# Kernel tuning notes

Measured on AMD Instinct MI355X. Metric: run time of the kernel, lower is better.

Reference implementation:

```python
import jax, jax.numpy as jnp
import numpy as np

B, S, HID, H = 2, 2048, 1024, 16
D = HID // H
LAMBDA_INIT = 0.8
GN_EPS = 1e-5


def setup_inputs() -> dict:
    rng = jax.random.key(0)
    ks = jax.random.split(rng, 12)
    w = 0.02
    return {
        "query": jax.random.normal(ks[0], (B, S, HID), dtype=jnp.float32),
        "key": jax.random.normal(ks[1], (B, S, HID), dtype=jnp.float32),
        "value": jax.random.normal(ks[2], (B, S, HID), dtype=jnp.float32),
        "attention_mask": jnp.ones((B, S), dtype=jnp.float32),
        # params ([in, out] layout; x @ W)
        "Wq": jax.random.normal(ks[3], (HID, H * D * 2), dtype=jnp.float32) * w,
        "Wk": jax.random.normal(ks[4], (HID, H * D * 2), dtype=jnp.float32) * w,
        "Wv": jax.random.normal(ks[5], (HID, H * D), dtype=jnp.float32) * w,
        "Wo": jax.random.normal(ks[6], (H * D, HID), dtype=jnp.float32) * w,
        "lam_q1": jax.random.normal(ks[7], (D,), dtype=jnp.float32),
        "lam_q2": jax.random.normal(ks[8], (D,), dtype=jnp.float32),
        "lam_k1": jax.random.normal(ks[9], (D,), dtype=jnp.float32),
        "lam_k2": jax.random.normal(ks[10], (D,), dtype=jnp.float32),
        "gn_weight": jnp.ones((H * D,), dtype=jnp.float32),
        "gn_bias": jnp.zeros((H * D,), dtype=jnp.float32),
    }


def reference(query, key, value, attention_mask, Wq, Wk, Wv, Wo,
              lam_q1, lam_q2, lam_k1, lam_k2, gn_weight, gn_bias):
    b, s, hid = query.shape
    h, d = H, hid // H
    rs = 1.0 / jnp.sqrt(jnp.asarray(d, query.dtype))

    q = (query @ Wq).reshape(b, s, h, 2 * d).transpose(0, 2, 1, 3)   # [b,h,s,2d]
    k = (key @ Wk).reshape(b, s, h, 2 * d).transpose(0, 2, 1, 3)
    v = (value @ Wv).reshape(b, s, h, d).transpose(0, 2, 1, 3)       # [b,h,s,d]

    Q1, Q2 = q[..., :d], q[..., d:]
    K1, K2 = k[..., :d], k[..., d:]
    s1 = jnp.einsum('bhqd,bhkd->bhqk', Q1, K1) * rs
    s2 = jnp.einsum('bhqd,bhkd->bhqk', Q2, K2) * rs

    # ALiBi bias: slopes[h] * (pos_q - pos_k), subtracted from scores
    pos = jnp.arange(s, dtype=query.dtype)
    slopes = 2.0 ** (-8.0 * jnp.arange(1, h + 1, dtype=query.dtype) / h)
    alibi = slopes[None, :, None, None] * (pos[:, None] - pos[None, :])[None, None]
    causal = jnp.triu(jnp.full((s, s), -1e9, dtype=query.dtype), k=1)[None, None]
    pad = (1.0 - attention_mask)[:, None, None, :] * -1e9
    add = -alibi + causal + pad

    w1 = jax.nn.softmax(s1 + add, axis=-1)
    w2 = jax.nn.softmax(s2 + add, axis=-1)

    lam = (jnp.exp(jnp.dot(lam_q1, lam_k1))
           - jnp.exp(jnp.dot(lam_q2, lam_k2)) + LAMBDA_INIT)
    dw = w1 - lam * w2

    attn = jnp.einsum('bhqk,bhkd->bhqd', dw, v).transpose(0, 2, 1, 3)  # [b,s,h,d]

    # GroupNorm(groups=h, channels=h*d) over [b, C, L]: per (b, head) normalize over (seq, d)
    mean = attn.mean(axis=(1, 3), keepdims=True)
    var = ((attn - mean) ** 2).mean(axis=(1, 3), keepdims=True)
    normed = (attn - mean) / jnp.sqrt(var + GN_EPS)
    normed = normed * gn_weight.reshape(1, 1, h, d) + gn_bias.reshape(1, 1, h, d)

    out = normed * (1.0 - LAMBDA_INIT)
    return out.reshape(b, s, h * d) @ Wo
```

## Files before the change

kernel.cpp:

```cpp
#include <hip/hip_runtime.h>
#include <cstdint>
#include <cstddef>

#define SQ 2048
#define NH 16
#define DH 64
#define HIDN 1024

typedef __attribute__((ext_vector_type(8))) short bf16x8;
typedef __attribute__((ext_vector_type(4))) float f32x4;
typedef __attribute__((ext_vector_type(2))) unsigned u32x2;

__device__ inline short f2b(float x) {
  union { float f; unsigned u; } un; un.f = x;
  unsigned r = un.u + 0x7fffu + ((un.u >> 16) & 1u);
  return (short)(r >> 16);
}

__device__ inline unsigned cvt_pk(float lo, float hi) {
  unsigned r;
  asm("v_cvt_pk_bf16_f32 %0, %1, %2" : "=v"(r) : "v"(lo), "v"(hi));
  return r;
}

__device__ inline f32x4 mfma16(u32x2 a, u32x2 b, f32x4 c) {
  asm("v_mfma_f32_16x16x16_bf16 %0, %1, %2, %0" : "+v"(c) : "v"(a), "v"(b));
  return c;
}

__device__ inline void gl_lds16(const void* g, void* l) {
  __builtin_amdgcn_global_load_lds(
      (const __attribute__((address_space(1))) void*)g,
      (__attribute__((address_space(3))) void*)l, 16, 0, 0);
}

__global__ __launch_bounds__(256) void qkv_to_bf16(const float4* __restrict__ q,
                                                   const float4* __restrict__ k,
                                                   const float4* __restrict__ v,
                                                   short4* __restrict__ out) {
  int i = blockIdx.x * 256 + threadIdx.x;
  const float4* src = (i < 1048576) ? q : ((i < 2097152) ? k : v);
  float4 val = src[i & 1048575];
  short4 o;
  o.x = f2b(val.x); o.y = f2b(val.y); o.z = f2b(val.z); o.w = f2b(val.w);
  out[i] = o;
}

__global__ __launch_bounds__(256) void wconv4(const float* __restrict__ Wq,
                                              const float* __restrict__ Wk,
                                              const float* __restrict__ Wv,
                                              const float* __restrict__ Wo,
                                              short* __restrict__ WqT, short* __restrict__ WkT,
                                              short* __restrict__ WvT, short* __restrict__ WoT) {
  __shared__ float t[32][33];
  int z = blockIdx.z;
  int N = (z < 2) ? 2048 : 1024;
  if (blockIdx.x * 32 >= N) return;
  const float* W = (z == 0) ? Wq : (z == 1) ? Wk : (z == 2) ? Wv : Wo;
  short* Wt = (z == 0) ? WqT : (z == 1) ? WkT : (z == 2) ? WvT : WoT;
  const int K = 1024;
  int n0 = blockIdx.x * 32, k0 = blockIdx.y * 32;
  int tx = threadIdx.x & 31, ty = threadIdx.x >> 5;
#pragma unroll
  for (int r = 0; r < 4; ++r)
    t[ty + r * 8][tx] = W[(size_t)(k0 + ty + r * 8) * N + n0 + tx];
  __syncthreads();
#pragma unroll
  for (int r = 0; r < 4; ++r)
    Wt[(size_t)(n0 + ty + r * 8) * K + k0 + tx] = f2b(t[tx][ty + r * 8]);
}

__global__ void lam_k(const float* __restrict__ q1, const float* __restrict__ q2,
                      const float* __restrict__ k1, const float* __restrict__ k2,
                      float* __restrict__ out) {
  int i = threadIdx.x;
  float d1 = q1[i] * k1[i], d2 = q2[i] * k2[i];
#pragma unroll
  for (int x = 1; x < 64; x <<= 1) { d1 += __shfl_xor(d1, x); d2 += __shfl_xor(d2, x); }
  if (i == 0) out[0] = __expf(d1) - __expf(d2) + 0.8f;
}

template <int MODE>
__global__ __launch_bounds__(256) void gemm_bt(const short* __restrict__ A,
                                               const short* __restrict__ Bt,
                                               void* __restrict__ Cout, int N, int K) {
  __shared__ __align__(16) short As[128 * 64];
  __shared__ __align__(16) short Bs[128 * 64];
  const int tid = threadIdx.x;
  const int lane = tid & 63, w = tid >> 6;
  const int l15 = lane & 15, lhi = lane >> 4;
  const int wr = w >> 1, wc = w & 1;
  const int m0 = blockIdx.y * 128, n0 = blockIdx.x * 128;

  f32x4 acc[4][4];
#pragma unroll
  for (int i = 0; i < 4; ++i)
#pragma unroll
    for (int j = 0; j < 4; ++j) acc[i][j] = (f32x4){0.f, 0.f, 0.f, 0.f};

  const short* Ag = A + (size_t)m0 * K;
  const short* Bg = Bt + (size_t)n0 * K;

  for (int k0 = 0; k0 < K; k0 += 64) {
#pragma unroll
    for (int it = 0; it < 4; ++it) {
      int idx = it * 256 + tid;
      int row = idx >> 3, c8 = (idx & 7) << 3;
      gl_lds16(Ag + (size_t)row * K + (k0 + c8), &As[idx << 3]);
      gl_lds16(Bg + (size_t)row * K + (k0 + c8), &Bs[idx << 3]);
    }
    __syncthreads();
#pragma unroll
    for (int kk = 0; kk < 64; kk += 32) {
      bf16x8 af[4], bfr[4];
#pragma unroll
      for (int mi = 0; mi < 4; ++mi)
        af[mi] = *(const bf16x8*)&As[(wr * 64 + mi * 16 + l15) * 64 + kk + lhi * 8];
#pragma unroll
      for (int ni = 0; ni < 4; ++ni)
        bfr[ni] = *(const bf16x8*)&Bs[(wc * 64 + ni * 16 + l15) * 64 + kk + lhi * 8];
#pragma unroll
      for (int mi = 0; mi < 4; ++mi)
#pragma unroll
        for (int ni = 0; ni < 4; ++ni)
          acc[mi][ni] = __builtin_amdgcn_mfma_f32_16x16x32_bf16(af[mi], bfr[ni], acc[mi][ni], 0, 0, 0);
    }
    __syncthreads();
  }

#pragma unroll
  for (int mi = 0; mi < 4; ++mi) {
#pragma unroll
    for (int ni = 0; ni < 4; ++ni) {
#pragma unroll
      for (int j = 0; j < 4; ++j) {
        int m = m0 + wr * 64 + mi * 16 + (lhi << 2) + j;
        int n = n0 + wc * 64 + ni * 16 + l15;
        float v = acc[mi][ni][j];
        if (MODE == 0) {
          ((float*)Cout)[(size_t)m * N + n] = v;
        } else if (MODE == 1) {
          int s = m & (SQ - 1), bb = m >> 11;
          int h = n >> 7, t = n & 127, path = t >> 6, tt = t & 63;
          ((short*)Cout)[((((size_t)(bb * NH + h) * 2 + path) * SQ + s) << 6) + tt] = f2b(v);
        } else {
          int s = m & (SQ - 1), bb = m >> 11;
          int h = n >> 6, t = n & 63;
          ((short*)Cout)[(((size_t)(bb * NH + h) << 6) + t) * SQ + s] = f2b(v);
        }
      }
    }
  }
}

__global__ __launch_bounds__(256) void diff_attn(
    const short* __restrict__ Qp, const short* __restrict__ Kp,
    const short* __restrict__ Vt, const float* __restrict__ maskp,
    const float* __restrict__ lamp, float* __restrict__ attn,
    float* __restrict__ part) {
  __shared__ __align__(16) short K1s[64 * 64];
  __shared__ __align__(16) short K2s[64 * 64];
  __shared__ __align__(16) short Vts[64 * 64];
  __shared__ float d_s[2048];
  __shared__ float red[8];

  const int bid = blockIdx.x;
  const int chunk = bid >> 8, c = bid & 255, sub = c >> 5, bh = c & 31;
  int qt;
  if (chunk == 0) qt = 31 - sub;
  else if (chunk == 1) qt = 16 + sub;
  else if (chunk == 2) qt = 15 - sub;
  else qt = sub;

  const int b = bh >> 4, h = bh & 15;
  const int tid = threadIdx.x, lane = tid & 63, w = tid >> 6;
  const int l15 = lane & 15, lhi = lane >> 4;
  const int sw7 = l15 & 7;
  const int u0 = (lhi ^ sw7) << 3, u1 = ((4 + lhi) ^ sw7) << 3;
  const int wq0 = qt * 64 + w * 16;
  const int q = wq0 + l15;
  const float slope = exp2f(-0.5f * (float)(h + 1));
  const float L2E = 1.44269504089f;
  const float SC = 0.125f * L2E;
  const float qb8 = slope * (float)q * L2E + 8.0f;

  for (int i = tid; i < 2048; i += 256)
    d_s[i] = (slope * (float)i + (1.0f - maskp[(b << 11) + i]) * (-1.0e9f)) * L2E;

  const short* Q1g = Qp + (((size_t)bh * 2 + 0) * SQ) * DH;
  const short* Q2g = Qp + (((size_t)bh * 2 + 1) * SQ) * DH;
  const short* K1g = Kp + (((size_t)bh * 2 + 0) * SQ) * DH;
  const short* K2g = Kp + (((size_t)bh * 2 + 1) * SQ) * DH;
  const short* Vtg = Vt + (size_t)bh * DH * SQ;

  bf16x8 aq[2][2];
#pragma unroll
  for (int kk = 0; kk < 2; ++kk) {
    aq[0][kk] = *(const bf16x8*)&Q1g[(size_t)q * DH + kk * 32 + lhi * 8];
    aq[1][kk] = *(const bf16x8*)&Q2g[(size_t)q * DH + kk * 32 + lhi * 8];
  }

  int ucf[4];
#pragma unroll
  for (int cf = 0; cf < 4; ++cf)
    ucf[cf] = (((2 * cf + (lhi >> 1)) ^ sw7) << 1) + (lhi & 1);

  f32x4 acc[2][4];
  float ll[2] = {0.f, 0.f};
#pragma unroll
  for (int p = 0; p < 2; ++p)
#pragma unroll
    for (int i = 0; i < 4; ++i) acc[p][i] = (f32x4){0.f, 0.f, 0.f, 0.f};

  for (int kt = 0; kt <= qt; ++kt) {
    const int k0 = kt * 64;
#pragma unroll
    for (int it = 0; it < 2; ++it) {
      int idx = it * 256 + tid;
      int row = idx >> 3, u = idx & 7;
      int us = (u ^ (row & 7)) << 3;
      gl_lds16(K1g + (size_t)(k0 + row) * DH + us, &K1s[idx << 3]);
      gl_lds16(K2g + (size_t)(k0 + row) * DH + us, &K2s[idx << 3]);
      gl_lds16(Vtg + (size_t)row * SQ + k0 + us, &Vts[idx << 3]);
    }
    __syncthreads();

    f32x4 dvq[4];
#pragma unroll
    for (int cf = 0; cf < 4; ++cf) {
      f32x4 dv = *(const f32x4*)&d_s[k0 + 16 * cf + 4 * lhi];
#pragma unroll
      for (int j = 0; j < 4; ++j) dvq[cf][j] = dv[j] - qb8;
    }
    const bool diag = (kt == qt);

    u32x2 pa[2][4];
#pragma unroll
    for (int p = 0; p < 2; ++p) {
      const short* Ks = (p == 0) ? K1s : K2s;
      f32x4 sv[4];
#pragma unroll
      for (int cf = 0; cf < 4; ++cf) {
        int rb = (cf * 16 + l15) << 6;
        f32x4 z = (f32x4){0.f, 0.f, 0.f, 0.f};
        bf16x8 ka = *(const bf16x8*)&Ks[rb + u0];
        bf16x8 kb = *(const bf16x8*)&Ks[rb + u1];
        sv[cf] = __builtin_amdgcn_mfma_f32_16x16x32_bf16(ka, aq[p][0], z, 0, 0, 0);
        sv[cf] = __builtin_amdgcn_mfma_f32_16x16x32_bf16(kb, aq[p][1], sv[cf], 0, 0, 0);
      }
      float rsum = 0.f;
#pragma unroll
      for (int cf = 0; cf < 4; ++cf) {
        float pv[4];
#pragma unroll
        for (int j = 0; j < 4; ++j) pv[j] = sv[cf][j] * SC + dvq[cf][j];
        if (diag) {
#pragma unroll
          for (int j = 0; j < 4; ++j) {
            int kc = k0 + 16 * cf + 4 * lhi + j;
            pv[j] = (kc > q) ? -1.0e9f : pv[j];
          }
        }
        float e0 = exp2f(pv[0]);
        float e1 = exp2f(pv[1]);
        float e2 = exp2f(pv[2]);
        float e3 = exp2f(pv[3]);
        rsum += (e0 + e1) + (e2 + e3);
        pa[p][cf][0] = cvt_pk(e0, e1);
        pa[p][cf][1] = cvt_pk(e2, e3);
      }
      ll[p] += rsum;
    }

#pragma unroll
    for (int df = 0; df < 4; ++df) {
      const u32x2* vrow = (const u32x2*)&Vts[(df * 16 + l15) << 6];
#pragma unroll
      for (int cf = 0; cf < 4; ++cf) {
        u32x2 vb = vrow[ucf[cf]];
        acc[0][df] = mfma16(pa[0][cf], vb, acc[0][df]);
        acc[1][df] = mfma16(pa[1][cf], vb, acc[1][df]);
      }
    }
    __syncthreads();
  }

#pragma unroll
  for (int p = 0; p < 2; ++p) {
    ll[p] += __shfl_xor(ll[p], 16);
    ll[p] += __shfl_xor(ll[p], 32);
  }
  float lamv = lamp[0];
  float li1 = 1.0f / ll[0], li2 = lamv / ll[1];
  float li1b[4], li2b[4];
#pragma unroll
  for (int j = 0; j < 4; ++j) {
    li1b[j] = __shfl(li1, (lhi << 2) + j);
    li2b[j] = __shfl(li2, (lhi << 2) + j);
  }
  float lsum = 0.f, lsq = 0.f;
#pragma unroll
  for (int df = 0; df < 4; ++df)
#pragma unroll
    for (int j = 0; j < 4; ++j) {
      int qq = wq0 + (lhi << 2) + j;
      float o = acc[0][df][j] * li1b[j] - acc[1][df][j] * li2b[j];
      attn[((size_t)b * SQ + qq) * HIDN + (h << 6) + (df << 4) + l15] = o;
      lsum += o; lsq += o * o;
    }
#pragma unroll
  for (int x = 1; x < 64; x <<= 1) {
    lsum += __shfl_xor(lsum, x);
    lsq += __shfl_xor(lsq, x);
  }
  if (lane == 0) { red[w] = lsum; red[4 + w] = lsq; }
  __syncthreads();
  if (tid == 0) {
    part[((size_t)bh * 32 + qt) * 2] = red[0] + red[1] + red[2] + red[3];
    part[((size_t)bh * 32 + qt) * 2 + 1] = red[4] + red[5] + red[6] + red[7];
  }
}

__global__ void stats_fin(const float* __restrict__ part, float* __restrict__ mi) {
  int bh = threadIdx.x;
  float s = 0.f, ss = 0.f;
  for (int t = 0; t < 32; ++t) {
    s += part[(bh * 32 + t) * 2];
    ss += part[(bh * 32 + t) * 2 + 1];
  }
  float n = (float)(SQ * DH);
  float mean = s / n;
  float var = ss / n - mean * mean;
  mi[bh * 2] = mean;
  mi[bh * 2 + 1] = rsqrtf(var + 1e-5f);
}

__global__ __launch_bounds__(256) void gn_apply(const float* __restrict__ attn,
                                                const float* __restrict__ mi,
                                                const float* __restrict__ gnw,
                                                const float* __restrict__ gnb,
                                                short* __restrict__ X) {
  size_t i = (size_t)blockIdx.x * 256 + threadIdx.x;
  size_t base = i << 2;
  int r = (int)(base >> 10);
  int c = (int)(base & 1023);
  int bh = ((r >> 11) << 4) + (c >> 6);
  float mean = mi[bh * 2], inv = mi[bh * 2 + 1];
  float4 a = *(const float4*)&attn[base];
  short4 o;
  o.x = f2b(((a.x - mean) * inv * gnw[c + 0] + gnb[c + 0]) * 0.2f);
  o.y = f2b(((a.y - mean) * inv * gnw[c + 1] + gnb[c + 1]) * 0.2f);
  o.z = f2b(((a.z - mean) * inv * gnw[c + 2] + gnb[c + 2]) * 0.2f);
  o.w = f2b(((a.w - mean) * inv * gnw[c + 3] + gnb[c + 3]) * 0.2f);
  *(short4*)&X[base] = o;
}

extern "C" void kernel_launch(void* const* d_in, const int* in_sizes, int n_in,
                              void* d_out, int out_size, void* d_ws, size_t ws_size,
                              hipStream_t stream) {
  const float* query = (const float*)d_in[0];
  const float* key = (const float*)d_in[1];
  const float* value = (const float*)d_in[2];
  const float* mask = (const float*)d_in[3];
  const float* Wq = (const float*)d_in[4];
  const float* Wk = (const float*)d_in[5];
  const float* Wv = (const float*)d_in[6];
  const float* Wo = (const float*)d_in[7];
  const float* lq1 = (const float*)d_in[8];
  const float* lq2 = (const float*)d_in[9];
  const float* lk1 = (const float*)d_in[10];
  const float* lk2 = (const float*)d_in[11];
  const float* gnw = (const float*)d_in[12];
  const float* gnb = (const float*)d_in[13];

  char* ws = (char*)d_ws;
  short* WqT = (short*)(ws + 0);
  short* WkT = (short*)(ws + 4194304);
  short* WvT = (short*)(ws + 8388608);
  short* WoT = (short*)(ws + 10485760);
  short* qb = (short*)(ws + 12582912);
  short* kb = (short*)(ws + 20971520);
  short* vb = (short*)(ws + 29360128);
  short* Qp = (short*)(ws + 37748736);
  short* Kp = (short*)(ws + 54525952);
  short* Vtb = (short*)(ws + 71303168);
  float* attn = (float*)(ws + 12582912);
  short* X = (short*)(ws + 29360128);
  float* part = (float*)(ws + 79691776);
  float* mi = (float*)(ws + 79699968);
  float* lam = (float*)(ws + 79700224);

  qkv_to_bf16<<<12288, 256, 0, stream>>>((const float4*)query, (const float4*)key,
                                         (const float4*)value, (short4*)qb);
  wconv4<<<dim3(64, 32, 4), 256, 0, stream>>>(Wq, Wk, Wv, Wo, WqT, WkT, WvT, WoT);
  lam_k<<<1, 64, 0, stream>>>(lq1, lq2, lk1, lk2, lam);

  gemm_bt<1><<<dim3(16, 32), 256, 0, stream>>>(qb, WqT, Qp, 2048, 1024);
  gemm_bt<1><<<dim3(16, 32), 256, 0, stream>>>(kb, WkT, Kp, 2048, 1024);
  gemm_bt<2><<<dim3(8, 32), 256, 0, stream>>>(vb, WvT, Vtb, 1024, 1024);

  diff_attn<<<dim3(1024), 256, 0, stream>>>(Qp, Kp, Vtb, mask, lam, attn, part);
  stats_fin<<<1, 32, 0, stream>>>(part, mi);
  gn_apply<<<4096, 256, 0, stream>>>(attn, mi, gnw, gnb, X);
  gemm_bt<0><<<dim3(8, 32), 256, 0, stream>>>(X, WoT, d_out, 1024, 1024);
}
```

Baseline: 219.6 us.

## Merge QKV projections into one launch and pair query stripes for causal balance

The three projection GEMMs are combined into a single launch using a z-dimension, and the output GEMM becomes its own non-templated kernel. The attention kernel now gives each block two 32-row query stripes, a and 63-a, handled by different wave pairs, so every block does about the same causal work. The GroupNorm partial-statistics buffer doubles to match. Waves on the shorter stripe still wait at each K/V tile barrier until the longer stripe finishes, so some waves sit idle during the tail of each block.

Measured after the change: 267.1 us. +21.6%, slower.

```diff
diff --git a/kernel.cpp b/kernel.cpp
--- a/kernel.cpp
+++ b/kernel.cpp
@@ -80,10 +80,17 @@
   if (i == 0) out[0] = __expf(d1) - __expf(d2) + 0.8f;
 }
 
-template <int MODE>
-__global__ __launch_bounds__(256) void gemm_bt(const short* __restrict__ A,
-                                               const short* __restrict__ Bt,
-                                               void* __restrict__ Cout, int N, int K) {
+__global__ __launch_bounds__(256) void proj3(const short* __restrict__ Abase,
+                                             const short* __restrict__ Btbase,
+                                             short* __restrict__ QKout,
+                                             short* __restrict__ Vtb) {
+  const int z = blockIdx.z;
+  if (z == 2 && blockIdx.x >= 8) return;
+  const int N = (z < 2) ? 2048 : 1024;
+  const int K = 1024;
+  const short* A = Abase + (size_t)z * 4194304;
+  const short* Bt = Btbase + (size_t)z * 2097152;
+
   __shared__ __align__(16) short As[128 * 64];
   __shared__ __align__(16) short Bs[128 * 64];
   const int tid = threadIdx.x;
@@ -137,20 +144,78 @@
         int m = m0 + wr * 64 + mi * 16 + (lhi << 2) + j;
         int n = n0 + wc * 64 + ni * 16 + l15;
         float v = acc[mi][ni][j];
-        if (MODE == 0) {
-          ((float*)Cout)[(size_t)m * N + n] = v;
-        } else if (MODE == 1) {
-          int s = m & (SQ - 1), bb = m >> 11;
+        int s = m & (SQ - 1), bb = m >> 11;
+        if (z < 2) {
           int h = n >> 7, t = n & 127, path = t >> 6, tt = t & 63;
-          ((short*)Cout)[((((size_t)(bb * NH + h) * 2 + path) * SQ + s) << 6) + tt] = f2b(v);
+          (QKout + (size_t)z * 8388608)
+              [((((size_t)(bb * NH + h) * 2 + path) * SQ + s) << 6) + tt] = f2b(v);
         } else {
-          int s = m & (SQ - 1), bb = m >> 11;
           int h = n >> 6, t = n & 63;
-          ((short*)Cout)[(((size_t)(bb * NH + h) << 6) + t) * SQ + s] = f2b(v);
+          Vtb[(((size_t)(bb * NH + h) << 6) + t) * SQ + s] = f2b(v);
         }
       }
     }
   }
+}
+
+__global__ __launch_bounds__(256) void gemm_out(const short* __restrict__ A,
+                                                const short* __restrict__ Bt,
+                                                float* __restrict__ Cout) {
+  const int N = 1024, K = 1024;
+  __shared__ __align__(16) short As[128 * 64];
+  __shared__ __align__(16) short Bs[128 * 64];
+  const int tid = threadIdx.x;
+  const int lane = tid & 63, w = tid >> 6;
+  const int l15 = lane & 15, lhi = lane >> 4;
+  const int wr = w >> 1, wc = w & 1;
+  const int m0 = blockIdx.y * 128, n0 = blockIdx.x * 128;
+
+  f32x4 acc[4][4];
+#pragma unroll
+  for (int i = 0; i < 4; ++i)
+#pragma unroll
+    for (int j = 0; j < 4; ++j) acc[i][j] = (f32x4){0.f, 0.f, 0.f, 0.f};
+
+  const short* Ag = A + (size_t)m0 * K;
+  const short* Bg = Bt + (size_t)n0 * K;
+
+  for (int k0 = 0; k0 < K; k0 += 64) {
+#pragma unroll
+    for (int it = 0; it < 4; ++it) {
+      int idx = it * 256 + tid;
+      int row = idx >> 3, c8 = (idx & 7) << 3;
+      gl_lds16(Ag + (size_t)row * K + (k0 + c8), &As[idx << 3]);
+      gl_lds16(Bg + (size_t)row * K + (k0 + c8), &Bs[idx << 3]);
+    }
+    __syncthreads();
+#pragma unroll
+    for (int kk = 0; kk < 64; kk += 32) {
+      bf16x8 af[4], bfr[4];
+#pragma unroll
+      for (int mi = 0; mi < 4; ++mi)
+        af[mi] = *(const bf16x8*)&As[(wr * 64 + mi * 16 + l15) * 64 + kk + lhi * 8];
+#pragma unroll
+      for (int ni = 0; ni < 4; ++ni)
+        bfr[ni] = *(const bf16x8*)&Bs[(wc * 64 + ni * 16 + l15) * 64 + kk + lhi * 8];
+#pragma unroll
+      for (int mi = 0; mi < 4; ++mi)
+#pragma unroll
+        for (int ni = 0; ni < 4; ++ni)
+          acc[mi][ni] = __builtin_amdgcn_mfma_f32_16x16x32_bf16(af[mi], bfr[ni], acc[mi][ni], 0, 0, 0);
+    }
+    __syncthreads();
+  }
+
+#pragma unroll
+  for (int mi = 0; mi < 4; ++mi)
+#pragma unroll
+    for (int ni = 0; ni < 4; ++ni)
+#pragma unroll
+      for (int j = 0; j < 4; ++j) {
+        int m = m0 + wr * 64 + mi * 16 + (lhi << 2) + j;
+        int n = n0 + wc * 64 + ni * 16 + l15;
+        Cout[(size_t)m * N + n] = acc[mi][ni][j];
+      }
 }
 
 __global__ __launch_bounds__(256) void diff_attn(
@@ -165,20 +230,21 @@
   __shared__ float red[8];
 
   const int bid = blockIdx.x;
-  const int chunk = bid >> 8, c = bid & 255, sub = c >> 5, bh = c & 31;
-  int qt;
-  if (chunk == 0) qt = 31 - sub;
-  else if (chunk == 1) qt = 16 + sub;
-  else if (chunk == 2) qt = 15 - sub;
-  else qt = sub;
+  const int chunk = bid >> 8, cc = bid & 255, sub = cc >> 5, bh = cc & 31;
+  const int a = chunk * 8 + sub;
 
   const int b = bh >> 4, h = bh & 15;
   const int tid = threadIdx.x, lane = tid & 63, w = tid >> 6;
   const int l15 = lane & 15, lhi = lane >> 4;
   const int sw7 = l15 & 7;
   const int u0 = (lhi ^ sw7) << 3, u1 = ((4 + lhi) ^ sw7) << 3;
-  const int wq0 = qt * 64 + w * 16;
+
+  const int st = (w >> 1) ? (63 - a) : a;
+  const int ktmax = st >> 1;
+  const int ktmaxB = (63 - a) >> 1;
+  const int wq0 = st * 32 + (w & 1) * 16;
   const int q = wq0 + l15;
+
   const float slope = exp2f(-0.5f * (float)(h + 1));
   const float L2E = 1.44269504089f;
   const float SC = 0.125f * L2E;
@@ -212,7 +278,7 @@
 #pragma unroll
     for (int i = 0; i < 4; ++i) acc[p][i] = (f32x4){0.f, 0.f, 0.f, 0.f};
 
-  for (int kt = 0; kt <= qt; ++kt) {
+  for (int kt = 0; kt <= ktmaxB; ++kt) {
     const int k0 = kt * 64;
 #pragma unroll
     for (int it = 0; it < 2; ++it) {
@@ -225,61 +291,63 @@
     }
     __syncthreads();
 
-    f32x4 dvq[4];
-#pragma unroll
-    for (int cf = 0; cf < 4; ++cf) {
-      f32x4 dv = *(const f32x4*)&d_s[k0 + 16 * cf + 4 * lhi];
-#pragma unroll
-      for (int j = 0; j < 4; ++j) dvq[cf][j] = dv[j] - qb8;
-    }
-    const bool diag = (kt == qt);
-
-    u32x2 pa[2][4];
-#pragma unroll
-    for (int p = 0; p < 2; ++p) {
-      const short* Ks = (p == 0) ? K1s : K2s;
-      f32x4 sv[4];
+    if (kt <= ktmax) {
+      f32x4 dvq[4];
 #pragma unroll
       for (int cf = 0; cf < 4; ++cf) {
-        int rb = (cf * 16 + l15) << 6;
-        f32x4 z = (f32x4){0.f, 0.f, 0.f, 0.f};
-        bf16x8 ka = *(const bf16x8*)&Ks[rb + u0];
-        bf16x8 kb = *(const bf16x8*)&Ks[rb + u1];
-        sv[cf] = __builtin_amdgcn_mfma_f32_16x16x32_bf16(ka, aq[p][0], z, 0, 0, 0);
-        sv[cf] = __builtin_amdgcn_mfma_f32_16x16x32_bf16(kb, aq[p][1], sv[cf], 0, 0, 0);
+        f32x4 dv = *(const f32x4*)&d_s[k0 + 16 * cf + 4 * lhi];
+#pragma unroll
+        for (int j = 0; j < 4; ++j) dvq[cf][j] = dv[j] - qb8;
       }
-      float rsum = 0.f;
-#pragma unroll
-      for (int cf = 0; cf < 4; ++cf) {
-        float pv[4];
-#pragma unroll
-        for (int j = 0; j < 4; ++j) pv[j] = sv[cf][j] * SC + dvq[cf][j];
-        if (diag) {
-#pragma unroll
-          for (int j = 0; j < 4; ++j) {
-            int kc = k0 + 16 * cf + 4 * lhi + j;
-            pv[j] = (kc > q) ? -1.0e9f : pv[j];
+      const bool diag = (kt == ktmax);
+
+      u32x2 pa[2][4];
+#pragma unroll
+      for (int p = 0; p < 2; ++p) {
+        const short* Ks = (p == 0) ? K1s : K2s;
+        f32x4 sv[4];
+#pragma unroll
+        for (int cf = 0; cf < 4; ++cf) {
+          int rb = (cf * 16 + l15) << 6;
+          f32x4 z = (f32x4){0.f, 0.f, 0.f, 0.f};
+          bf16x8 ka = *(const bf16x8*)&Ks[rb + u0];
+          bf16x8 kb = *(const bf16x8*)&Ks[rb + u1];
+          sv[cf] = __builtin_amdgcn_mfma_f32_16x16x32_bf16(ka, aq[p][0], z, 0, 0, 0);
+          sv[cf] = __builtin_amdgcn_mfma_f32_16x16x32_bf16(kb, aq[p][1], sv[cf], 0, 0, 0);
+        }
+        float rsum = 0.f;
+#pragma unroll
+        for (int cf = 0; cf < 4; ++cf) {
+          float pv[4];
+#pragma unroll
+          for (int j = 0; j < 4; ++j) pv[j] = sv[cf][j] * SC + dvq[cf][j];
+          if (diag) {
+#pragma unroll
+            for (int j = 0; j < 4; ++j) {
+              int kc = k0 + 16 * cf + 4 * lhi + j;
+              pv[j] = (kc > q) ? -1.0e9f : pv[j];
+            }
           }
+          float e0 = exp2f(pv[0]);
+          float e1 = exp2f(pv[1]);
+          float e2 = exp2f(pv[2]);
+          float e3 = exp2f(pv[3]);
+          rsum += (e0 + e1) + (e2 + e3);
+          pa[p][cf][0] = cvt_pk(e0, e1);
+          pa[p][cf][1] = cvt_pk(e2, e3);
         }
-        float e0 = exp2f(pv[0]);
-        float e1 = exp2f(pv[1]);
-        float e2 = exp2f(pv[2]);
-        float e3 = exp2f(pv[3]);
-        rsum += (e0 + e1) + (e2 + e3);
-        pa[p][cf][0] = cvt_pk(e0, e1);
-        pa[p][cf][1] = cvt_pk(e2, e3);
+        ll[p] += rsum;
       }
-      ll[p] += rsum;
-    }
-
-#pragma unroll
-    for (int df = 0; df < 4; ++df) {
-      const u32x2* vrow = (const u32x2*)&Vts[(df * 16 + l15) << 6];
-#pragma unroll
-      for (int cf = 0; cf < 4; ++cf) {
-        u32x2 vb = vrow[ucf[cf]];
-        acc[0][df] = mfma16(pa[0][cf], vb, acc[0][df]);
-        acc[1][df] = mfma16(pa[1][cf], vb, acc[1][df]);
+
+#pragma unroll
+      for (int df = 0; df < 4; ++df) {
+        const u32x2* vrow = (const u32x2*)&Vts[(df * 16 + l15) << 6];
+#pragma unroll
+        for (int cf = 0; cf < 4; ++cf) {
+          u32x2 vb = vrow[ucf[cf]];
+          acc[0][df] = mfma16(pa[0][cf], vb, acc[0][df]);
+          acc[1][df] = mfma16(pa[1][cf], vb, acc[1][df]);
+        }
       }
     }
     __syncthreads();
@@ -316,17 +384,19 @@
   if (lane == 0) { red[w] = lsum; red[4 + w] = lsq; }
   __syncthreads();
   if (tid == 0) {
-    part[((size_t)bh * 32 + qt) * 2] = red[0] + red[1] + red[2] + red[3];
-    part[((size_t)bh * 32 + qt) * 2 + 1] = red[4] + red[5] + red[6] + red[7];
+    part[((size_t)bh * 64 + a) * 2] = red[0] + red[1];
+    part[((size_t)bh * 64 + a) * 2 + 1] = red[4] + red[5];
+    part[((size_t)bh * 64 + (63 - a)) * 2] = red[2] + red[3];
+    part[((size_t)bh * 64 + (63 - a)) * 2 + 1] = red[6] + red[7];
   }
 }
 
 __global__ void stats_fin(const float* __restrict__ part, float* __restrict__ mi) {
   int bh = threadIdx.x;
   float s = 0.f, ss = 0.f;
-  for (int t = 0; t < 32; ++t) {
-    s += part[(bh * 32 + t) * 2];
-    ss += part[(bh * 32 + t) * 2 + 1];
+  for (int t = 0; t < 64; ++t) {
+    s += part[(bh * 64 + t) * 2];
+    ss += part[(bh * 64 + t) * 2 + 1];
   }
   float n = (float)(SQ * DH);
   float mean = s / n;
@@ -375,32 +445,28 @@
 
   char* ws = (char*)d_ws;
   short* WqT = (short*)(ws + 0);
-  short* WkT = (short*)(ws + 4194304);
-  short* WvT = (short*)(ws + 8388608);
   short* WoT = (short*)(ws + 10485760);
   short* qb = (short*)(ws + 12582912);
-  short* kb = (short*)(ws + 20971520);
-  short* vb = (short*)(ws + 29360128);
   short* Qp = (short*)(ws + 37748736);
-  short* Kp = (short*)(ws + 54525952);
   short* Vtb = (short*)(ws + 71303168);
   float* attn = (float*)(ws + 12582912);
   short* X = (short*)(ws + 29360128);
   float* part = (float*)(ws + 79691776);
-  float* mi = (float*)(ws + 79699968);
-  float* lam = (float*)(ws + 79700224);
+  float* mi = (float*)(ws + 79708160);
+  float* lam = (float*)(ws + 79708416);
+  short* WkT = (short*)(ws + 4194304);
+  short* WvT = (short*)(ws + 8388608);
+  short* Kp = (short*)(ws + 54525952);
 
   qkv_to_bf16<<<12288, 256, 0, stream>>>((const float4*)query, (const float4*)key,
                                          (const float4*)value, (short4*)qb);
   wconv4<<<dim3(64, 32, 4), 256, 0, stream>>>(Wq, Wk, Wv, Wo, WqT, WkT, WvT, WoT);
   lam_k<<<1, 64, 0, stream>>>(lq1, lq2, lk1, lk2, lam);
 
-  gemm_bt<1><<<dim3(16, 32), 256, 0, stream>>>(qb, WqT, Qp, 2048, 1024);
-  gemm_bt<1><<<dim3(16, 32), 256, 0, stream>>>(kb, WkT, Kp, 2048, 1024);
-  gemm_bt<2><<<dim3(8, 32), 256, 0, stream>>>(vb, WvT, Vtb, 1024, 1024);
+  proj3<<<dim3(16, 32, 3), 256, 0, stream>>>(qb, WqT, Qp, Vtb);
 
   diff_attn<<<dim3(1024), 256, 0, stream>>>(Qp, Kp, Vtb, mask, lam, attn, part);
   stats_fin<<<1, 32, 0, stream>>>(part, mi);
   gn_apply<<<4096, 256, 0, stream>>>(attn, mi, gnw, gnb, X);
-  gemm_bt<0><<<dim3(8, 32), 256, 0, stream>>>(X, WoT, d_out, 1024, 1024);
-}
+  gemm_out<<<dim3(8, 32), 256, 0, stream>>>(X, WoT, (float*)d_out);
+}
```
